# Kernel optimization log

Measured on AMD Instinct MI355X. Metric: run time of the kernel, lower is better.

## Reference

```python
import jax, jax.numpy as jnp
import numpy as np

D_MODEL = 1024
N_HEADS = 16
DIM_HEAD = 64
NUM_MEM_KV = 16
INNER = N_HEADS * DIM_HEAD  # 1024


def setup_inputs() -> dict:
    key = jax.random.key(0)
    ks = jax.random.split(key, 8)
    s = 0.02
    x = jax.random.normal(ks[0], (2, 2048, D_MODEL), dtype=jnp.float32)
    Wq = jax.random.normal(ks[1], (D_MODEL, INNER), dtype=jnp.float32) * s
    Wkv = jax.random.normal(ks[2], (D_MODEL, 2 * INNER), dtype=jnp.float32) * s
    Wo = jax.random.normal(ks[3], (INNER, D_MODEL), dtype=jnp.float32) * s
    pre_proj = jax.random.normal(ks[4], (N_HEADS, N_HEADS), dtype=jnp.float32)
    post_proj = jax.random.normal(ks[5], (N_HEADS, N_HEADS), dtype=jnp.float32)
    mem_k = jax.random.normal(ks[6], (N_HEADS, NUM_MEM_KV, DIM_HEAD), dtype=jnp.float32)
    mem_v = jax.random.normal(ks[7], (N_HEADS, NUM_MEM_KV, DIM_HEAD), dtype=jnp.float32)
    return {"x": x, "Wq": Wq, "Wkv": Wkv, "Wo": Wo,
            "pre_proj": pre_proj, "post_proj": post_proj,
            "mem_k": mem_k, "mem_v": mem_v}


def reference(x, Wq, Wkv, Wo, pre_proj, post_proj, mem_k, mem_v):
    b, n, _ = x.shape
    scale = DIM_HEAD ** -0.5
    # projections (no bias)
    q = x @ Wq                              # [b, n, inner]
    kv = x @ Wkv                            # self-attention: context = x
    k, v = jnp.split(kv, 2, axis=-1)
    split_heads = lambda t: t.reshape(b, n, N_HEADS, DIM_HEAD).transpose(0, 2, 1, 3)
    q, k, v = split_heads(q), split_heads(k), split_heads(v)  # [b, h, n, d]
    # prepend memory key/values along kv axis
    mk = jnp.broadcast_to(mem_k[None], (b, N_HEADS, NUM_MEM_KV, DIM_HEAD))
    mv = jnp.broadcast_to(mem_v[None], (b, N_HEADS, NUM_MEM_KV, DIM_HEAD))
    k = jnp.concatenate([mk, k], axis=2)    # [b, h, j, d], j = mem + n
    v = jnp.concatenate([mv, v], axis=2)
    dots = jnp.einsum('bhid,bhjd->bhij', q, k) * scale
    # pre-softmax talking-heads mixing
    dots = jnp.einsum('bhij,hk->bkij', dots, pre_proj)
    # causal mask with mem-kv offset: triu(ones(i,j), j-i+1)
    i, j = dots.shape[-2], dots.shape[-1]
    causal = jnp.triu(jnp.ones((i, j), dtype=bool), k=j - i + 1)
    mask_value = jnp.finfo(dots.dtype).min
    dots = jnp.where(causal[None, None], mask_value, dots)
    attn = jax.nn.softmax(dots, axis=-1)
    # post-softmax talking-heads mixing
    attn = jnp.einsum('bhij,hk->bkij', attn, post_proj)
    out = jnp.einsum('bhij,bhjd->bhid', attn, v)   # [b, h, n, d]
    out = out.transpose(0, 2, 1, 3).reshape(b, n, INNER)
    return out @ Wo                                # [b, n, d_model]
```

## Files before the change

kernel.cpp:

```cpp
#include <hip/hip_runtime.h>


typedef __attribute__((ext_vector_type(8))) short short8;
typedef __attribute__((ext_vector_type(4))) float floatx4;

#define MFMA16(a, b, c) __builtin_amdgcn_mfma_f32_16x16x32_bf16(a, b, c, 0, 0, 0)
#define BARLDS() __asm__ volatile("s_waitcnt lgkmcnt(0)\n\ts_barrier" ::: "memory")

static __device__ __forceinline__ unsigned short f2bf(float f) {
  union { float f; unsigned u; } v; v.f = f;
  unsigned r = v.u + 0x7fffu + ((v.u >> 16) & 1u);
  return (unsigned short)(r >> 16);
}
static __device__ __forceinline__ float bf2f(unsigned short h) {
  union { unsigned u; float f; } v; v.u = ((unsigned)h) << 16;
  return v.f;
}

union S8U { short8 v; unsigned short u[8]; };

__global__ __launch_bounds__(256) void conv_bf16(const float* __restrict__ src,
                                                 unsigned short* __restrict__ dst,
                                                 int n8) {
  int tid = blockIdx.x * 256 + threadIdx.x;
  if (tid >= n8) return;
  const float4* s = (const float4*)src + (size_t)tid * 2;
  float4 a = s[0], b = s[1];
  S8U o;
  o.u[0] = f2bf(a.x); o.u[1] = f2bf(a.y); o.u[2] = f2bf(a.z); o.u[3] = f2bf(a.w);
  o.u[4] = f2bf(b.x); o.u[5] = f2bf(b.y); o.u[6] = f2bf(b.z); o.u[7] = f2bf(b.w);
  *(short8*)(dst + (size_t)tid * 8) = o.v;
}

__global__ __launch_bounds__(256) void transW(const float* __restrict__ src, int Ncols,
                                              unsigned short* __restrict__ dst, int dstRowOff) {
  __shared__ float sw[32][33];
  int n0 = blockIdx.x * 32, k0 = blockIdx.y * 32;
  int t = threadIdx.x;
  int lk = t >> 3, n4 = (t & 7) * 4;
  const float* s = src + (size_t)(k0 + lk) * Ncols + n0 + n4;
  sw[lk][n4 + 0] = s[0]; sw[lk][n4 + 1] = s[1];
  sw[lk][n4 + 2] = s[2]; sw[lk][n4 + 3] = s[3];
  __syncthreads();
  int ln = t >> 3, k4 = (t & 7) * 4;
  unsigned o0 = f2bf(sw[k4 + 0][ln]) | ((unsigned)f2bf(sw[k4 + 1][ln]) << 16);
  unsigned o1 = f2bf(sw[k4 + 2][ln]) | ((unsigned)f2bf(sw[k4 + 3][ln]) << 16);
  uint2 pk; pk.x = o0; pk.y = o1;
  *(uint2*)(dst + (size_t)(dstRowOff + n0 + ln) * 1024 + k0 + k4) = pk;
}

__global__ __launch_bounds__(256) void gemm_bt(const unsigned short* __restrict__ A,
                                               const unsigned short* __restrict__ BT,
                                               unsigned short* __restrict__ Cb,
                                               float* __restrict__ Cf,
                                               int M, int N, int K, int f32out) {
  __shared__ unsigned short Al[128 * 40];
  __shared__ unsigned short Bl[128 * 40];
  const int t = threadIdx.x;
  const int w = t >> 6, lane = t & 63;
  const int quad = lane >> 4, l16 = lane & 15;
  const int mb = blockIdx.x * 128, nb = blockIdx.y * 128;
  const int m0 = (w >> 1) * 64, n0 = (w & 1) * 64;
  const int srow = t >> 1, scol = (t & 1) * 16;
  const unsigned short* Ag = A + (size_t)(mb + srow) * K + scol;
  const unsigned short* Bg = BT + (size_t)(nb + srow) * K + scol;
  unsigned short* Aw = Al + srow * 40 + scol;
  unsigned short* Bw = Bl + srow * 40 + scol;

  floatx4 acc[4][4];
#pragma unroll
  for (int i = 0; i < 4; i++)
#pragma unroll
    for (int j = 0; j < 4; j++) acc[i][j] = (floatx4){0.f, 0.f, 0.f, 0.f};

  short8 a0 = *(const short8*)(Ag);
  short8 a1 = *(const short8*)(Ag + 8);
  short8 b0 = *(const short8*)(Bg);
  short8 b1 = *(const short8*)(Bg + 8);

  for (int kk = 0; kk < K; kk += 32) {
    __syncthreads();
    *(short8*)(Aw) = a0; *(short8*)(Aw + 8) = a1;
    *(short8*)(Bw) = b0; *(short8*)(Bw + 8) = b1;
    __syncthreads();
    if (kk + 32 < K) {
      a0 = *(const short8*)(Ag + kk + 32);
      a1 = *(const short8*)(Ag + kk + 40);
      b0 = *(const short8*)(Bg + kk + 32);
      b1 = *(const short8*)(Bg + kk + 40);
    }
    short8 af[4], bf[4];
#pragma unroll
    for (int s = 0; s < 4; s++) {
      af[s] = *(const short8*)(Al + (m0 + s * 16 + l16) * 40 + quad * 8);
      bf[s] = *(const short8*)(Bl + (n0 + s * 16 + l16) * 40 + quad * 8);
    }
#pragma unroll
    for (int mt = 0; mt < 4; mt++)
#pragma unroll
      for (int nt = 0; nt < 4; nt++) acc[mt][nt] = MFMA16(af[mt], bf[nt], acc[mt][nt]);
  }
#pragma unroll
  for (int mt = 0; mt < 4; mt++)
#pragma unroll
    for (int nt = 0; nt < 4; nt++)
#pragma unroll
      for (int r = 0; r < 4; r++) {
        size_t row = mb + m0 + mt * 16 + quad * 4 + r;
        size_t col = nb + n0 + nt * 16 + l16;
        if (f32out) Cf[row * N + col] = acc[mt][nt][r];
        else Cb[row * N + col] = f2bf(acc[mt][nt][r]);
      }
}

__global__ __launch_bounds__(256) void fill_K(const unsigned short* __restrict__ qkv,
                                              const float* __restrict__ mem_k,
                                              unsigned short* __restrict__ Kw) {
  int tid = blockIdx.x * 256 + threadIdx.x;
  if (tid >= 2 * 16 * 2064 * 8) return;
  int d0 = (tid & 7) * 8;
  int j = (tid >> 3) % 2064;
  int h = ((tid >> 3) / 2064) & 15;
  int b = (tid >> 3) / (2064 * 16);
  S8U o;
  if (j < 16) {
    const float* s = mem_k + ((size_t)(h * 16 + j) * 64 + d0);
#pragma unroll
    for (int c = 0; c < 8; c++) o.u[c] = f2bf(s[c]);
  } else {
    o.v = *(const short8*)(qkv + (size_t)(b * 2048 + j - 16) * 3072 + 1024 + h * 64 + d0);
  }
  *(short8*)(Kw + ((size_t)(b * 16 + h) * 2064 + j) * 64 + d0) = o.v;
}

__global__ __launch_bounds__(256) void fill_Vt(const unsigned short* __restrict__ qkv,
                                               const float* __restrict__ mem_v,
                                               unsigned short* __restrict__ Vt) {
  __shared__ float sv[16][65];
  int jt = blockIdx.x, h = blockIdx.y, b = blockIdx.z;
  int t = threadIdx.x;
  int j = t >> 4, d0 = (t & 15) * 4;
  int jg = jt * 16 + j;
  float v0, v1, v2, v3;
  if (jg < 16) {
    const float* s = mem_v + ((size_t)(h * 16 + jg) * 64 + d0);
    v0 = s[0]; v1 = s[1]; v2 = s[2]; v3 = s[3];
  } else {
    const unsigned short* s = qkv + (size_t)(b * 2048 + jg - 16) * 3072 + 2048 + h * 64 + d0;
    v0 = bf2f(s[0]); v1 = bf2f(s[1]); v2 = bf2f(s[2]); v3 = bf2f(s[3]);
  }
  sv[j][d0 + 0] = v0; sv[j][d0 + 1] = v1; sv[j][d0 + 2] = v2; sv[j][d0 + 3] = v3;
  __syncthreads();
  int d = t >> 2, j4 = (t & 3) * 4;
  unsigned o0 = f2bf(sv[j4 + 0][d]) | ((unsigned)f2bf(sv[j4 + 1][d]) << 16);
  unsigned o1 = f2bf(sv[j4 + 2][d]) | ((unsigned)f2bf(sv[j4 + 3][d]) << 16);
  uint2 pk; pk.x = o0; pk.y = o1;
  *(uint2*)(Vt + ((size_t)(b * 16 + h) * 64 + d) * 2064 + jt * 16 + j4) = pk;
}

__global__ __launch_bounds__(1024) void attn_stats(const unsigned short* __restrict__ qkv,
                                                   const unsigned short* __restrict__ Kw,
                                                   const float* __restrict__ pre,
                                                   float* __restrict__ l_ws) {
  const int c = blockIdx.x, it = blockIdx.y, b = blockIdx.z;
  const int i0 = it * 64;
  const int jmax = i0 + 80;
  const int jc0 = c * 160;
  if (jc0 >= jmax) return;
  const int jend = min(jmax, jc0 + 160);
  const int niter = (jend - jc0 + 31) >> 5;

  __shared__ unsigned short S_lds[64 * 520];

  const int tid = threadIdx.x, w = tid >> 6, lane = tid & 63;
  const int quad = lane >> 4, l16 = lane & 15;
  const int hoff = (quad < 2) ? quad * 8 : 0;

  short8 qa[4][2];
#pragma unroll
  for (int s = 0; s < 4; s++) {
    const unsigned short* p =
        qkv + (size_t)(b * 2048 + i0 + s * 16 + l16) * 3072 + w * 64 + quad * 8;
    qa[s][0] = *(const short8*)p;
    qa[s][1] = *(const short8*)(p + 32);
  }
  short8 preA;
#pragma unroll
  for (int jj = 0; jj < 8; jj++) {
    int h = quad * 8 + jj;
    preA[jj] = (short)((quad < 2) ? f2bf(pre[h * 16 + l16] * 0.125f) : 0);
  }
  const unsigned short* Kb = Kw + (size_t)(b * 16 + w) * 2064 * 64;

  float l_loc[4][4];
#pragma unroll
  for (int i4 = 0; i4 < 4; i4++)
#pragma unroll
    for (int r = 0; r < 4; r++) l_loc[i4][r] = 0.f;

  short8 kf[2][2];
#pragma unroll
  for (int jt = 0; jt < 2; jt++) {
    int jr = min(jc0 + jt * 16 + l16, 2063);
    const unsigned short* kp = Kb + (size_t)jr * 64 + quad * 8;
    kf[jt][0] = *(const short8*)kp;
    kf[jt][1] = *(const short8*)(kp + 32);
  }

  for (int n = 0; n < niter; n++) {
    const int j0 = jc0 + n * 32;
#pragma unroll
    for (int jt = 0; jt < 2; jt++)
#pragma unroll
      for (int s = 0; s < 4; s++) {
        floatx4 a = (floatx4){0.f, 0.f, 0.f, 0.f};
        a = MFMA16(qa[s][0], kf[jt][0], a);
        a = MFMA16(qa[s][1], kf[jt][1], a);
#pragma unroll
        for (int r = 0; r < 4; r++)
          S_lds[(s * 16 + quad * 4 + r) * 520 + (jt * 16 + l16) * 16 + w] = f2bf(a[r]);
      }
    if (n + 1 < niter) {
      const int j0n = j0 + 32;
#pragma unroll
      for (int jt = 0; jt < 2; jt++) {
        int jr = min(j0n + jt * 16 + l16, 2063);
        const unsigned short* kp = Kb + (size_t)jr * 64 + quad * 8;
        kf[jt][0] = *(const short8*)kp;
        kf[jt][1] = *(const short8*)(kp + 32);
      }
    }
    BARLDS();
#pragma unroll
    for (int u = 0; u < 8; u++) {
      const int iloc = u >> 1, jt = u & 1, ii = w * 4 + iloc;
      const short8 bb = *(const short8*)(S_lds + ii * 520 + (jt * 16 + l16) * 16 + hoff);
      floatx4 sp = (floatx4){0.f, 0.f, 0.f, 0.f};
      sp = MFMA16(preA, bb, sp);
      const int jg = j0 + jt * 16 + l16;
      if (jg <= i0 + ii + 16) {
#pragma unroll
        for (int r = 0; r < 4; r++) l_loc[iloc][r] += __expf(sp[r]);
      }
    }
    if (n + 1 < niter) BARLDS();
  }
#pragma unroll
  for (int iloc = 0; iloc < 4; iloc++)
#pragma unroll
    for (int r = 0; r < 4; r++) {
      float v = l_loc[iloc][r];
      v += __shfl_xor(v, 1);
      v += __shfl_xor(v, 2);
      v += __shfl_xor(v, 4);
      v += __shfl_xor(v, 8);
      if (l16 == 0)
        atomicAdd(l_ws + ((size_t)(b * 2048 + i0 + w * 4 + iloc) * 16 + quad * 4 + r), v);
    }
}

__global__ __launch_bounds__(1024) void attn_av(const unsigned short* __restrict__ qkv,
                                                const unsigned short* __restrict__ Kw,
                                                const unsigned short* __restrict__ Vt,
                                                const float* __restrict__ pre,
                                                const float* __restrict__ post,
                                                const float* __restrict__ l_ws,
                                                float* __restrict__ O_ws) {
  const int c = blockIdx.x, it = blockIdx.y, b = blockIdx.z;
  const int i0 = it * 32;
  const int jmax = i0 + 48;
  const int jc0 = c * 160;
  if (jc0 >= jmax) return;
  const int jend = min(jmax, jc0 + 160);
  const int niter = (jend - jc0 + 31) >> 5;

  __shared__ unsigned short S_lds[32 * 520];
  __shared__ unsigned short Pp_lds[16 * 1288];

  const int tid = threadIdx.x, w = tid >> 6, lane = tid & 63;
  const int quad = lane >> 4, l16 = lane & 15;
  const int hoff = (quad < 2) ? quad * 8 : 0;
  const int srcA = (quad * 32 + l16) & 63;
  const int srcB = (srcA + 16) & 63;

  short8 qa[2][2];
#pragma unroll
  for (int s = 0; s < 2; s++) {
    const unsigned short* p =
        qkv + (size_t)(b * 2048 + i0 + s * 16 + l16) * 3072 + w * 64 + quad * 8;
    qa[s][0] = *(const short8*)p;
    qa[s][1] = *(const short8*)(p + 32);
  }
  short8 preA, postA;
#pragma unroll
  for (int jj = 0; jj < 8; jj++) {
    int h = quad * 8 + jj;
    float pv = 0.f, qv = 0.f;
    if (quad < 2) { pv = pre[h * 16 + l16] * 0.125f; qv = post[h * 16 + l16]; }
    preA[jj] = (short)f2bf(pv);
    postA[jj] = (short)f2bf(qv);
  }
  float rl[2][4];
#pragma unroll
  for (int iloc = 0; iloc < 2; iloc++)
#pragma unroll
    for (int r = 0; r < 4; r++)
      rl[iloc][r] = 1.0f / l_ws[(size_t)(b * 2048 + i0 + w * 2 + iloc) * 16 + quad * 4 + r];

  floatx4 oacc[2][4];
#pragma unroll
  for (int g = 0; g < 2; g++)
#pragma unroll
    for (int d = 0; d < 4; d++) oacc[g][d] = (floatx4){0.f, 0.f, 0.f, 0.f};

  const unsigned short* Kb = Kw + (size_t)(b * 16 + w) * 2064 * 64;
  const unsigned short* Vb = Vt + (size_t)(b * 16 + w) * 64 * 2064;

  short8 kf[2][2];
#pragma unroll
  for (int jt = 0; jt < 2; jt++) {
    int jr = min(jc0 + jt * 16 + l16, 2063);
    const unsigned short* kp = Kb + (size_t)jr * 64 + quad * 8;
    kf[jt][0] = *(const short8*)kp;
    kf[jt][1] = *(const short8*)(kp + 32);
  }

  for (int n = 0; n < niter; n++) {
    const int j0 = jc0 + n * 32;
    short8 vf[4];
    {
      const int jc = min(j0 + quad * 8, 2056);
#pragma unroll
      for (int d = 0; d < 4; d++)
        vf[d] = *(const short8*)(Vb + (size_t)(d * 16 + l16) * 2064 + jc);
    }
#pragma unroll
    for (int jt = 0; jt < 2; jt++)
#pragma unroll
      for (int s = 0; s < 2; s++) {
        floatx4 a = (floatx4){0.f, 0.f, 0.f, 0.f};
        a = MFMA16(qa[s][0], kf[jt][0], a);
        a = MFMA16(qa[s][1], kf[jt][1], a);
#pragma unroll
        for (int r = 0; r < 4; r++)
          S_lds[(s * 16 + quad * 4 + r) * 520 + (jt * 16 + l16) * 16 + w] = f2bf(a[r]);
      }
    if (n + 1 < niter) {
      const int j0n = j0 + 32;
#pragma unroll
      for (int jt = 0; jt < 2; jt++) {
        int jr = min(j0n + jt * 16 + l16, 2063);
        const unsigned short* kp = Kb + (size_t)jr * 64 + quad * 8;
        kf[jt][0] = *(const short8*)kp;
        kf[jt][1] = *(const short8*)(kp + 32);
      }
    }
    BARLDS();
#pragma unroll
    for (int u = 0; u < 4; u++) {
      const int iloc = u >> 1, jt = u & 1, ii = w * 2 + iloc;
      const int sc = ii * 520 + (jt * 16 + l16) * 16;
      const short8 bb = *(const short8*)(S_lds + sc + hoff);
      floatx4 sp = (floatx4){0.f, 0.f, 0.f, 0.f};
      sp = MFMA16(preA, bb, sp);
      const int jg = j0 + jt * 16 + l16;
      const bool keep = jg <= (i0 + ii + 16);
      float p0 = keep ? __expf(sp[0]) * rl[iloc][0] : 0.f;
      float p1 = keep ? __expf(sp[1]) * rl[iloc][1] : 0.f;
      float p2 = keep ? __expf(sp[2]) * rl[iloc][2] : 0.f;
      float p3 = keep ? __expf(sp[3]) * rl[iloc][3] : 0.f;
      unsigned w01 = (unsigned)f2bf(p0) | ((unsigned)f2bf(p1) << 16);
      unsigned w23 = (unsigned)f2bf(p2) | ((unsigned)f2bf(p3) << 16);
      union { unsigned u32[4]; short8 v; } pfu;
      pfu.u32[0] = __shfl(w01, srcA, 64);
      pfu.u32[1] = __shfl(w23, srcA, 64);
      pfu.u32[2] = __shfl(w01, srcB, 64);
      pfu.u32[3] = __shfl(w23, srcB, 64);
      floatx4 pp = (floatx4){0.f, 0.f, 0.f, 0.f};
      pp = MFMA16(postA, pfu.v, pp);
#pragma unroll
      for (int r = 0; r < 4; r++)
        Pp_lds[(quad * 4 + r) * 1288 + ii * 40 + jt * 16 + l16] = f2bf(pp[r]);
    }
    BARLDS();
#pragma unroll
    for (int g = 0; g < 2; g++) {
      const short8 paf = *(const short8*)(Pp_lds + w * 1288 + (g * 16 + l16) * 40 + quad * 8);
#pragma unroll
      for (int d = 0; d < 4; d++) oacc[g][d] = MFMA16(paf, vf[d], oacc[g][d]);
    }
  }
#pragma unroll
  for (int g = 0; g < 2; g++)
#pragma unroll
    for (int d = 0; d < 4; d++)
#pragma unroll
      for (int r = 0; r < 4; r++)
        atomicAdd(O_ws + (size_t)(b * 2048 + i0 + g * 16 + quad * 4 + r) * 1024 +
                      w * 64 + d * 16 + l16,
                  oacc[g][d][r]);
}

extern "C" void kernel_launch(void* const* d_in, const int* in_sizes, int n_in,
                              void* d_out, int out_size, void* d_ws, size_t ws_size,
                              hipStream_t stream) {
  (void)in_sizes; (void)n_in; (void)out_size; (void)ws_size;
  const float* x     = (const float*)d_in[0];
  const float* Wq    = (const float*)d_in[1];
  const float* Wkv   = (const float*)d_in[2];
  const float* Wo    = (const float*)d_in[3];
  const float* pre   = (const float*)d_in[4];
  const float* post  = (const float*)d_in[5];
  const float* mem_k = (const float*)d_in[6];
  const float* mem_v = (const float*)d_in[7];
  float* out = (float*)d_out;
  char* ws = (char*)d_ws;

  unsigned short* xb     = (unsigned short*)(ws);
  unsigned short* WbT    = (unsigned short*)(ws + 8388608);
  float*          O_ws   = (float*)(ws);
  unsigned short* qkv    = (unsigned short*)(ws + 16777216);
  unsigned short* WoT    = (unsigned short*)(ws + 16777216);
  unsigned short* Kw     = (unsigned short*)(ws + 41943040);
  unsigned short* Vt     = (unsigned short*)(ws + 50397184);
  float*          l_ws   = (float*)(ws + 58851328);
  unsigned short* attn_b = (unsigned short*)(ws + 58851328);

  conv_bf16<<<2048, 256, 0, stream>>>(x, xb, 524288);
  transW<<<dim3(32, 32), 256, 0, stream>>>(Wq, 1024, WbT, 0);
  transW<<<dim3(64, 32), 256, 0, stream>>>(Wkv, 2048, WbT, 1024);
  gemm_bt<<<dim3(32, 24), 256, 0, stream>>>(xb, WbT, qkv, nullptr, 4096, 3072, 1024, 0);
  fill_K<<<2064, 256, 0, stream>>>(qkv, mem_k, Kw);
  fill_Vt<<<dim3(129, 16, 2), 256, 0, stream>>>(qkv, mem_v, Vt);
  hipMemsetAsync(O_ws, 0, 16777216, stream);
  hipMemsetAsync(l_ws, 0, 262144, stream);
  attn_stats<<<dim3(13, 32, 2), 1024, 0, stream>>>(qkv, Kw, pre, l_ws);
  attn_av<<<dim3(13, 64, 2), 1024, 0, stream>>>(qkv, Kw, Vt, pre, post, l_ws, O_ws);
  conv_bf16<<<2048, 256, 0, stream>>>(O_ws, attn_b, 524288);
  transW<<<dim3(32, 32), 256, 0, stream>>>(Wo, 1024, WoT, 0);
  gemm_bt<<<dim3(32, 8), 256, 0, stream>>>(attn_b, WoT, nullptr, out, 4096, 1024, 1024, 1);
}
```

Before: 401.3 us.

## Double-buffer score LDS in attn_stats and halve query tile to 32 rows

```diff
diff --git a/kernel.cpp b/kernel.cpp
--- a/kernel.cpp
+++ b/kernel.cpp
@@ -158,27 +158,68 @@
   *(uint2*)(Vt + ((size_t)(b * 16 + h) * 64 + d) * 2064 + jt * 16 + j4) = pk;
 }
 
+
+#define ST_LOADK(KF, J0)                                                      \
+  { _Pragma("unroll") for (int jt = 0; jt < 2; jt++) {                        \
+      int jr = min((J0) + jt * 16 + l16, 2063);                               \
+      const unsigned short* kp = Kb + (size_t)jr * 64 + quad * 8;             \
+      KF[jt][0] = *(const short8*)kp;                                         \
+      KF[jt][1] = *(const short8*)(kp + 32);                                  \
+  } }
+
+#define ST_QK(SDST, KF)                                                      \
+  { _Pragma("unroll") for (int jt = 0; jt < 2; jt++)                         \
+      _Pragma("unroll") for (int s = 0; s < 2; s++) {                        \
+        floatx4 a = (floatx4){0.f, 0.f, 0.f, 0.f};                           \
+        a = MFMA16(qa[s][0], KF[jt][0], a);                                  \
+        a = MFMA16(qa[s][1], KF[jt][1], a);                                  \
+        _Pragma("unroll") for (int r = 0; r < 4; r++)                        \
+          (SDST)[(s * 16 + quad * 4 + r) * 520 + (jt * 16 + l16) * 16 + w] = \
+              f2bf(a[r]);                                                    \
+  } }
+
+#define ST_BODY(SCUR, SOTH, KF_USE, KF_LOAD)                                 \
+  { const int j0 = jc0 + n * 32;                                             \
+    _Pragma("unroll") for (int u = 0; u < 4; u++) {                          \
+      const int iloc = u >> 1, jt = u & 1, ii = w * 2 + iloc;                \
+      const short8 bb =                                                      \
+          *(const short8*)((SCUR) + ii * 520 + (jt * 16 + l16) * 16 + hoff); \
+      floatx4 sp = (floatx4){0.f, 0.f, 0.f, 0.f};                            \
+      sp = MFMA16(preA, bb, sp);                                             \
+      const int jg = j0 + jt * 16 + l16;                                     \
+      if (jg <= i0 + ii + 16) {                                              \
+        _Pragma("unroll") for (int r = 0; r < 4; r++)                        \
+          l_loc[iloc][r] += __expf(sp[r]);                                   \
+      }                                                                      \
+    }                                                                        \
+    if (n + 1 < niter) ST_QK(SOTH, KF_USE);                                  \
+    if (n + 2 < niter) ST_LOADK(KF_LOAD, jc0 + (n + 2) * 32);                \
+    if (n + 1 < niter) BARLDS();                                             \
+  }
+
 __global__ __launch_bounds__(1024) void attn_stats(const unsigned short* __restrict__ qkv,
                                                    const unsigned short* __restrict__ Kw,
                                                    const float* __restrict__ pre,
                                                    float* __restrict__ l_ws) {
   const int c = blockIdx.x, it = blockIdx.y, b = blockIdx.z;
-  const int i0 = it * 64;
-  const int jmax = i0 + 80;
+  const int i0 = it * 32;
+  const int jmax = i0 + 48;
   const int jc0 = c * 160;
   if (jc0 >= jmax) return;
   const int jend = min(jmax, jc0 + 160);
   const int niter = (jend - jc0 + 31) >> 5;
 
-  __shared__ unsigned short S_lds[64 * 520];
+  __shared__ unsigned short S_lds[2][32 * 520];
 
   const int tid = threadIdx.x, w = tid >> 6, lane = tid & 63;
   const int quad = lane >> 4, l16 = lane & 15;
   const int hoff = (quad < 2) ? quad * 8 : 0;
-
-  short8 qa[4][2];
-#pragma unroll
-  for (int s = 0; s < 4; s++) {
+  unsigned short* const S0 = S_lds[0];
+  unsigned short* const S1 = S_lds[1];
+
+  short8 qa[2][2];
+#pragma unroll
+  for (int s = 0; s < 2; s++) {
     const unsigned short* p =
         qkv + (size_t)(b * 2048 + i0 + s * 16 + l16) * 3072 + w * 64 + quad * 8;
     qa[s][0] = *(const short8*)p;
@@ -192,61 +233,28 @@
   }
   const unsigned short* Kb = Kw + (size_t)(b * 16 + w) * 2064 * 64;
 
-  float l_loc[4][4];
-#pragma unroll
-  for (int i4 = 0; i4 < 4; i4++)
+  float l_loc[2][4];
+#pragma unroll
+  for (int i4 = 0; i4 < 2; i4++)
 #pragma unroll
     for (int r = 0; r < 4; r++) l_loc[i4][r] = 0.f;
 
-  short8 kf[2][2];
-#pragma unroll
-  for (int jt = 0; jt < 2; jt++) {
-    int jr = min(jc0 + jt * 16 + l16, 2063);
-    const unsigned short* kp = Kb + (size_t)jr * 64 + quad * 8;
-    kf[jt][0] = *(const short8*)kp;
-    kf[jt][1] = *(const short8*)(kp + 32);
-  }
-
-  for (int n = 0; n < niter; n++) {
-    const int j0 = jc0 + n * 32;
-#pragma unroll
-    for (int jt = 0; jt < 2; jt++)
-#pragma unroll
-      for (int s = 0; s < 4; s++) {
-        floatx4 a = (floatx4){0.f, 0.f, 0.f, 0.f};
-        a = MFMA16(qa[s][0], kf[jt][0], a);
-        a = MFMA16(qa[s][1], kf[jt][1], a);
-#pragma unroll
-        for (int r = 0; r < 4; r++)
-          S_lds[(s * 16 + quad * 4 + r) * 520 + (jt * 16 + l16) * 16 + w] = f2bf(a[r]);
-      }
-    if (n + 1 < niter) {
-      const int j0n = j0 + 32;
-#pragma unroll
-      for (int jt = 0; jt < 2; jt++) {
-        int jr = min(j0n + jt * 16 + l16, 2063);
-        const unsigned short* kp = Kb + (size_t)jr * 64 + quad * 8;
-        kf[jt][0] = *(const short8*)kp;
-        kf[jt][1] = *(const short8*)(kp + 32);
-      }
-    }
-    BARLDS();
-#pragma unroll
-    for (int u = 0; u < 8; u++) {
-      const int iloc = u >> 1, jt = u & 1, ii = w * 4 + iloc;
-      const short8 bb = *(const short8*)(S_lds + ii * 520 + (jt * 16 + l16) * 16 + hoff);
-      floatx4 sp = (floatx4){0.f, 0.f, 0.f, 0.f};
-      sp = MFMA16(preA, bb, sp);
-      const int jg = j0 + jt * 16 + l16;
-      if (jg <= i0 + ii + 16) {
-#pragma unroll
-        for (int r = 0; r < 4; r++) l_loc[iloc][r] += __expf(sp[r]);
-      }
-    }
-    if (n + 1 < niter) BARLDS();
-  }
-#pragma unroll
-  for (int iloc = 0; iloc < 4; iloc++)
+  short8 kfA[2][2], kfB[2][2];
+  ST_LOADK(kfA, jc0);
+  ST_QK(S0, kfA);
+  if (niter > 1) ST_LOADK(kfB, jc0 + 32);
+  BARLDS();
+
+  int n = 0;
+  while (true) {
+    ST_BODY(S0, S1, kfB, kfA);
+    if (++n == niter) break;
+    ST_BODY(S1, S0, kfA, kfB);
+    if (++n == niter) break;
+  }
+
+#pragma unroll
+  for (int iloc = 0; iloc < 2; iloc++)
 #pragma unroll
     for (int r = 0; r < 4; r++) {
       float v = l_loc[iloc][r];
@@ -255,7 +263,7 @@
       v += __shfl_xor(v, 4);
       v += __shfl_xor(v, 8);
       if (l16 == 0)
-        atomicAdd(l_ws + ((size_t)(b * 2048 + i0 + w * 4 + iloc) * 16 + quad * 4 + r), v);
+        atomicAdd(l_ws + ((size_t)(b * 2048 + i0 + w * 2 + iloc) * 16 + quad * 4 + r), v);
     }
 }
 
@@ -434,7 +442,7 @@
   fill_Vt<<<dim3(129, 16, 2), 256, 0, stream>>>(qkv, mem_v, Vt);
   hipMemsetAsync(O_ws, 0, 16777216, stream);
   hipMemsetAsync(l_ws, 0, 262144, stream);
-  attn_stats<<<dim3(13, 32, 2), 1024, 0, stream>>>(qkv, Kw, pre, l_ws);
+  attn_stats<<<dim3(13, 64, 2), 1024, 0, stream>>>(qkv, Kw, pre, l_ws);
   attn_av<<<dim3(13, 64, 2), 1024, 0, stream>>>(qkv, Kw, Vt, pre, post, l_ws, O_ws);
   conv_bf16<<<2048, 256, 0, stream>>>(O_ws, attn_b, 524288);
   transW<<<dim3(32, 32), 256, 0, stream>>>(Wo, 1024, WoT, 0);
```

Result: no change. 406.1 us (+1.2%).
